# Kernel optimization log

Measured on AMD Instinct MI355X. Metric: run time of the kernel, lower is better.

## Reference

```python
import jax, jax.numpy as jnp
from jax import lax
import numpy as np

B, C, H, W = 16, 16, 256, 256
NOISE = 4
HID = 128
CDIM = 64
NCLS = 32
STEP_SIZE = 0.1
FIN = 3 * C + NOISE  # 52


def _lin(k, fin, fout, scale=None):
    # torch nn.Linear default init: U(-1/sqrt(fin), 1/sqrt(fin))
    s = (1.0 / np.sqrt(fin)) if scale is None else scale
    kw, kb = jax.random.split(k)
    w = jax.random.uniform(kw, (fin, fout), minval=-s, maxval=s, dtype=jnp.float32)
    b = jax.random.uniform(kb, (fout,), minval=-s, maxval=s, dtype=jnp.float32)
    return w, b


def setup_inputs() -> dict:
    key = jax.random.key(0)
    ks = jax.random.split(key, 8)
    x = jax.random.normal(ks[0], (B, C, H, W), dtype=jnp.float32)
    cond = jax.random.randint(ks[1], (B,), 0, NCLS)
    embed_tab = jax.random.normal(ks[2], (NCLS, CDIM), dtype=jnp.float32)
    film1_w, film1_b = _lin(ks[3], CDIM, 2 * HID)
    film2_w, film2_b = _lin(ks[4], CDIM, 2 * HID)
    fc1_w, fc1_b = _lin(ks[5], FIN, HID)
    fc2_w, fc2_b = _lin(ks[6], HID, HID)
    # original zero-inits fc3 (degenerate); use small random instead
    fc3_w, fc3_b = _lin(ks[7], HID, C, scale=0.02)
    return dict(x=x, cond=cond, embed_tab=embed_tab,
                film1_w=film1_w, film1_b=film1_b,
                film2_w=film2_w, film2_b=film2_b,
                fc1_w=fc1_w, fc1_b=fc1_b, fc2_w=fc2_w, fc2_b=fc2_b,
                fc3_w=fc3_w, fc3_b=fc3_b, n_steps=1)


def _dwconv(v, k2d):
    # depthwise 3x3 'same' conv, NCHW / OIHW
    kern = jnp.broadcast_to(k2d, (C, 1, 3, 3)).astype(v.dtype)
    return lax.conv_general_dilated(v, kern, (1, 1), 'SAME', feature_group_count=C)


def reference(x, cond, embed_tab, film1_w, film1_b, film2_w, film2_b,
              fc1_w, fc1_b, fc2_w, fc2_b, fc3_w, fc3_b, n_steps):
    sobel_x = jnp.array([[-1., 0., 1.], [-2., 0., 2.], [-1., 0., 1.]], jnp.float32)
    sobel_y = sobel_x.T
    emb = embed_tab[cond]                       # [B, CDIM]
    f1 = emb @ film1_w + film1_b                # [B, 2*HID]
    gamma1, beta1 = f1[:, :HID], f1[:, HID:]
    f2 = emb @ film2_w + film2_b
    gamma2, beta2 = f2[:, :HID], f2[:, HID:]
    for t in range(n_steps):
        gx = _dwconv(x, sobel_x)
        gy = _dwconv(x, sobel_y)
        noise = jax.random.normal(jax.random.fold_in(jax.random.key(1), t),
                                  (B, NOISE, H, W), dtype=x.dtype)
        feats = jnp.concatenate([x, gx, gy, noise], axis=1).transpose(0, 2, 3, 1)  # [B,H,W,FIN]
        h = jax.nn.relu(feats @ fc1_w + fc1_b)
        h = gamma1[:, None, None, :] * h + beta1[:, None, None, :]
        h = jax.nn.relu(h @ fc2_w + fc2_b)
        h = gamma2[:, None, None, :] * h + beta2[:, None, None, :]
        dx = (h @ fc3_w + fc3_b).transpose(0, 3, 1, 2)  # [B,C,H,W]
        dx = jnp.clip(dx, -10.0, 10.0)
        x = x + dx * STEP_SIZE
    return x
```

## Files before the change

### kernel.cpp

```cpp
#include <hip/hip_runtime.h>
#include <hip/hip_bf16.h>

using short8 = __attribute__((ext_vector_type(8))) short;
using f32x4  = __attribute__((ext_vector_type(4))) float;

constexpr int Bn = 16, Cc = 16, Hh = 256, Ww = 256;
constexpr int NOISEC = 4, HID = 128, CDIM = 64;
constexpr unsigned NTOT = (unsigned)Bn * NOISEC * Hh * Ww;
constexpr unsigned HALF = NTOT / 2;

__host__ __device__ __forceinline__ unsigned rotl(unsigned x, int d) {
    return (x << d) | (x >> (32 - d));
}

__host__ __device__ __forceinline__ void tf2x32(unsigned k0, unsigned k1,
                                                unsigned c0, unsigned c1,
                                                unsigned& o0, unsigned& o1) {
    unsigned k2 = k0 ^ k1 ^ 0x1BD11BDAu;
    unsigned x0 = c0 + k0, x1 = c1 + k1;
    x0 += x1; x1 = rotl(x1, 13); x1 ^= x0;
    x0 += x1; x1 = rotl(x1, 15); x1 ^= x0;
    x0 += x1; x1 = rotl(x1, 26); x1 ^= x0;
    x0 += x1; x1 = rotl(x1, 6);  x1 ^= x0;
    x0 += k1; x1 += k2 + 1u;
    x0 += x1; x1 = rotl(x1, 17); x1 ^= x0;
    x0 += x1; x1 = rotl(x1, 29); x1 ^= x0;
    x0 += x1; x1 = rotl(x1, 16); x1 ^= x0;
    x0 += x1; x1 = rotl(x1, 24); x1 ^= x0;
    x0 += k2; x1 += k0 + 2u;
    x0 += x1; x1 = rotl(x1, 13); x1 ^= x0;
    x0 += x1; x1 = rotl(x1, 15); x1 ^= x0;
    x0 += x1; x1 = rotl(x1, 26); x1 ^= x0;
    x0 += x1; x1 = rotl(x1, 6);  x1 ^= x0;
    x0 += k0; x1 += k1 + 3u;
    x0 += x1; x1 = rotl(x1, 17); x1 ^= x0;
    x0 += x1; x1 = rotl(x1, 29); x1 ^= x0;
    x0 += x1; x1 = rotl(x1, 16); x1 ^= x0;
    x0 += x1; x1 = rotl(x1, 24); x1 ^= x0;
    x0 += k1; x1 += k2 + 4u;
    x0 += x1; x1 = rotl(x1, 13); x1 ^= x0;
    x0 += x1; x1 = rotl(x1, 15); x1 ^= x0;
    x0 += x1; x1 = rotl(x1, 26); x1 ^= x0;
    x0 += x1; x1 = rotl(x1, 6);  x1 ^= x0;
    x0 += k2; x1 += k0 + 5u;
    o0 = x0; o1 = x1;
}

__device__ __forceinline__ float erfinv_f(float x) {
    float w = -log1pf(-x * x);
    float p;
    if (w < 5.0f) {
        w = w - 2.5f;
        p = 2.81022636e-08f;
        p = fmaf(p, w, 3.43273939e-07f);
        p = fmaf(p, w, -3.5233877e-06f);
        p = fmaf(p, w, -4.39150654e-06f);
        p = fmaf(p, w, 0.00021858087f);
        p = fmaf(p, w, -0.00125372503f);
        p = fmaf(p, w, -0.00417768164f);
        p = fmaf(p, w, 0.246640727f);
        p = fmaf(p, w, 1.50140941f);
    } else {
        w = sqrtf(w) - 3.0f;
        p = -0.000200214257f;
        p = fmaf(p, w, 0.000100950558f);
        p = fmaf(p, w, 0.00134934322f);
        p = fmaf(p, w, -0.00367342844f);
        p = fmaf(p, w, 0.00573950773f);
        p = fmaf(p, w, -0.0076224613f);
        p = fmaf(p, w, 0.00943887047f);
        p = fmaf(p, w, 1.00167406f);
        p = fmaf(p, w, 2.83297682f);
    }
    return p * x;
}

__device__ __forceinline__ float noise_val(unsigned j, unsigned fk0, unsigned fk1) {
    unsigned i = (j < HALF) ? j : (j - HALF);
    unsigned o0, o1;
    tf2x32(fk0, fk1, i, i + HALF, o0, o1);
    unsigned bits = (j < HALF) ? o0 : o1;
    unsigned fb = (bits >> 9) | 0x3F800000u;
    float f = __uint_as_float(fb) - 1.0f;
    const float lo = -0.99999994f;
    float u = f * 2.0f + lo;
    u = fmaxf(lo, u);
    return 1.4142135381698608f * erfinv_f(u);
}

__device__ __forceinline__ ushort f2bf(float f) {
    unsigned u = __float_as_uint(f);
    unsigned r = (u + 0x7FFFu + ((u >> 16) & 1u)) >> 16;
    return (ushort)r;
}

__device__ __forceinline__ unsigned cvtpk(float lo, float hi) {
    unsigned r;
    asm volatile("v_cvt_pk_bf16_f32 %0, %1, %2" : "=v"(r) : "v"(lo), "v"(hi));
    return r;
}

__device__ __forceinline__ unsigned rsw(int row) {
    return ((unsigned)((row ^ (row >> 4)) & 15)) << 4;
}

__global__ void film_kernel(const int* __restrict__ cond,
                            const float* __restrict__ embed,
                            const float* __restrict__ f1w, const float* __restrict__ f1b,
                            const float* __restrict__ f2w, const float* __restrict__ f2b,
                            float* __restrict__ film) {
    int b = blockIdx.x;
    int j = threadIdx.x;
    __shared__ float emb[CDIM];
    if (j < CDIM) emb[j] = embed[(size_t)cond[b] * CDIM + j];
    __syncthreads();
    float a1 = f1b[j], a2 = f2b[j];
    for (int c = 0; c < CDIM; ++c) {
        float e = emb[c];
        a1 += e * f1w[c * 2 * HID + j];
        a2 += e * f2w[c * 2 * HID + j];
    }
    int which = j >> 7;
    int idx = j & 127;
    float* fb_ = film + (size_t)b * 4 * HID;
    fb_[which * HID + idx] = a1;
    fb_[(2 + which) * HID + idx] = a2;
}

__global__ void prep_weights(const float* __restrict__ fc1w,
                             const float* __restrict__ fc2w,
                             const float* __restrict__ fc3w,
                             ushort* __restrict__ w1t, ushort* __restrict__ w2t,
                             ushort* __restrict__ w3t) {
    int i = blockIdx.x * 256 + threadIdx.x;
    if (i < 128 * 64) {
        int j = i >> 6, k = i & 63;
        w1t[i] = (k < 52) ? f2bf(fc1w[k * HID + j]) : (ushort)0;
    } else if (i < 8192 + 128 * 128) {
        int m = i - 8192;
        int j = m >> 7, k = m & 127;
        w2t[m] = f2bf(fc2w[k * HID + j]);
    } else if (i < 8192 + 16384 + 16 * 128) {
        int m = i - 24576;
        int c = m >> 7, k = m & 127;
        w3t[m] = f2bf(fc3w[k * Cc + c]);
    }
}

__global__ __launch_bounds__(256, 2)
void nca_mfma(const float* __restrict__ x,
              const ushort* __restrict__ w1t, const ushort* __restrict__ w2t,
              const ushort* __restrict__ w3t,
              const float* __restrict__ fc1b, const float* __restrict__ fc2b,
              const float* __restrict__ fc3b, const float* __restrict__ film,
              float* __restrict__ out, unsigned fk0, unsigned fk1) {
    __shared__ __align__(16) unsigned char Hb[256 * 256];

    const int blk = blockIdx.x, b = blk >> 8, y = blk & 255;
    const int t = threadIdx.x;
    const float* xb = x + (size_t)b * Cc * Hh * Ww;

    {
        const int q  = t & 63;
        const int cq = t >> 6;
        const int px0 = q * 4;
        const bool okm = (y > 0), okp = (y < Hh - 1);
        const bool ql = (q > 0), qr = (q < 63);

        float vx[4][4], vgx[4][4], vgy[4][4];
        #pragma unroll
        for (int cc = 0; cc < 4; ++cc) {
            const int c = cq * 4 + cc;
            const float* base = xb + ((size_t)c * Hh + (size_t)y) * Ww + px0;
            const float4 fz = {0.f, 0.f, 0.f, 0.f};
            float4 rm = okm ? *(const float4*)(base - Ww) : fz;
            float4 rc = *(const float4*)(base);
            float4 rp = okp ? *(const float4*)(base + Ww) : fz;
            float mL = __shfl_up(rm.w, 1),  mR = __shfl_down(rm.x, 1);
            float cL = __shfl_up(rc.w, 1),  cR = __shfl_down(rc.x, 1);
            float pL = __shfl_up(rp.w, 1),  pR = __shfl_down(rp.x, 1);
            if (!ql) { mL = 0.f; cL = 0.f; pL = 0.f; }
            if (!qr) { mR = 0.f; cR = 0.f; pR = 0.f; }
            float am[6] = {mL, rm.x, rm.y, rm.z, rm.w, mR};
            float ac[6] = {cL, rc.x, rc.y, rc.z, rc.w, cR};
            float ap[6] = {pL, rp.x, rp.y, rp.z, rp.w, pR};
            #pragma unroll
            for (int i = 0; i < 4; ++i) {
                float a0 = am[i], a1 = am[i + 1], a2 = am[i + 2];
                float b0 = ac[i], b1 = ac[i + 1], b2 = ac[i + 2];
                float e0 = ap[i], e1 = ap[i + 1], e2 = ap[i + 2];
                vx[cc][i]  = b1;
                vgx[cc][i] = (a2 + 2.f * b2 + e2) - (a0 + 2.f * b0 + e0);
                vgy[cc][i] = (e0 + 2.f * e1 + e2) - (a0 + 2.f * a1 + a2);
            }
        }
        #pragma unroll
        for (int i = 0; i < 4; ++i) {
            const int row = px0 + i;
            const unsigned sw = rsw(row);
            unsigned char* rowp = Hb + row * 256;
            uint2 u;
            u.x = cvtpk(vx[0][i], vx[1][i]);  u.y = cvtpk(vx[2][i], vx[3][i]);
            *(uint2*)(rowp + ((128u + 8u * cq) ^ sw)) = u;
            u.x = cvtpk(vgx[0][i], vgx[1][i]); u.y = cvtpk(vgx[2][i], vgx[3][i]);
            *(uint2*)(rowp + ((160u + 8u * cq) ^ sw)) = u;
            u.x = cvtpk(vgy[0][i], vgy[1][i]); u.y = cvtpk(vgy[2][i], vgy[3][i]);
            *(uint2*)(rowp + ((192u + 8u * cq) ^ sw)) = u;
        }
        unsigned nbase = (((unsigned)(b * NOISEC + cq) * Hh + (unsigned)y) * Ww) + (unsigned)px0;
        #pragma unroll
        for (int i = 0; i < 4; ++i) {
            float nz = noise_val(nbase + (unsigned)i, fk0, fk1);
            const int row = px0 + i;
            const unsigned sw = rsw(row);
            *(ushort*)(Hb + row * 256 + (((224u ^ sw) + 2u * cq))) = f2bf(nz);
        }
        if (cq == 0) {
            #pragma unroll
            for (int i = 0; i < 4; ++i) {
                const int row = px0 + i;
                const unsigned sw = rsw(row);
                *(uint2*)(Hb + row * 256 + ((232u & 15u) + (224u ^ sw))) = (uint2){0u, 0u};
                *(uint4*)(Hb + row * 256 + (240u ^ sw)) = (uint4){0u, 0u, 0u, 0u};
            }
        }
    }
    __syncthreads();

    const int lane = t & 63, wv = t >> 6;
    const int q = lane >> 4, p = lane & 15;
    const int nt0 = wv * 4;

    unsigned swn[4];
    #pragma unroll
    for (int n = 0; n < 4; ++n) swn[n] = rsw((nt0 + n) * 16 + p);

    f32x4 acc[8][4];

    #pragma unroll
    for (int m = 0; m < 8; ++m)
        #pragma unroll
        for (int n = 0; n < 4; ++n) acc[m][n] = (f32x4){0.f, 0.f, 0.f, 0.f};

    #pragma unroll
    for (int ks = 0; ks < 2; ++ks) {
        short8 Bf[4];
        #pragma unroll
        for (int n = 0; n < 4; ++n) {
            int row = (nt0 + n) * 16 + p;
            Bf[n] = *(const short8*)(Hb + row * 256 +
                                     (((unsigned)(128 + ks * 64 + q * 16)) ^ swn[n]));
        }
        #pragma unroll
        for (int m = 0; m < 8; ++m) {
            short8 Af = *(const short8*)((const unsigned char*)w1t +
                                         (m * 16 + p) * 128 + ks * 64 + q * 16);
            #pragma unroll
            for (int n = 0; n < 4; ++n)
                acc[m][n] = __builtin_amdgcn_mfma_f32_16x16x32_bf16(Af, Bf[n], acc[m][n], 0, 0, 0);
        }
    }
    const float* flm = film + (size_t)b * 4 * HID;
    #pragma unroll
    for (int m = 0; m < 8; ++m) {
        int j0 = m * 16 + q * 4;
        float4 cb = *(const float4*)(fc1b + j0);
        float4 G  = *(const float4*)(flm + 0 * HID + j0);
        float4 Be = *(const float4*)(flm + 1 * HID + j0);
        #pragma unroll
        for (int n = 0; n < 4; ++n) {
            int row = (nt0 + n) * 16 + p;
            f32x4 a = acc[m][n];
            float v0 = G.x * fmaxf(a[0] + cb.x, 0.f) + Be.x;
            float v1 = G.y * fmaxf(a[1] + cb.y, 0.f) + Be.y;
            float v2 = G.z * fmaxf(a[2] + cb.z, 0.f) + Be.z;
            float v3 = G.w * fmaxf(a[3] + cb.w, 0.f) + Be.w;
            uint2 u2; u2.x = cvtpk(v0, v1); u2.y = cvtpk(v2, v3);
            *(uint2*)(Hb + row * 256 + (((unsigned)(m * 32 + q * 8)) ^ swn[n])) = u2;
        }
    }

    #pragma unroll
    for (int m = 0; m < 8; ++m)
        #pragma unroll
        for (int n = 0; n < 4; ++n) acc[m][n] = (f32x4){0.f, 0.f, 0.f, 0.f};

    #pragma unroll
    for (int ks = 0; ks < 4; ++ks) {
        short8 Bf[4];
        #pragma unroll
        for (int n = 0; n < 4; ++n) {
            int row = (nt0 + n) * 16 + p;
            Bf[n] = *(const short8*)(Hb + row * 256 +
                                     (((unsigned)(ks * 64 + q * 16)) ^ swn[n]));
        }
        #pragma unroll
        for (int m = 0; m < 8; ++m) {
            short8 Af = *(const short8*)((const unsigned char*)w2t +
                                         (m * 16 + p) * 256 + ks * 64 + q * 16);
            #pragma unroll
            for (int n = 0; n < 4; ++n)
                acc[m][n] = __builtin_amdgcn_mfma_f32_16x16x32_bf16(Af, Bf[n], acc[m][n], 0, 0, 0);
        }
    }
    #pragma unroll
    for (int m = 0; m < 8; ++m) {
        int j0 = m * 16 + q * 4;
        float4 cb = *(const float4*)(fc2b + j0);
        float4 G  = *(const float4*)(flm + 2 * HID + j0);
        float4 Be = *(const float4*)(flm + 3 * HID + j0);
        #pragma unroll
        for (int n = 0; n < 4; ++n) {
            int row = (nt0 + n) * 16 + p;
            f32x4 a = acc[m][n];
            float v0 = G.x * fmaxf(a[0] + cb.x, 0.f) + Be.x;
            float v1 = G.y * fmaxf(a[1] + cb.y, 0.f) + Be.y;
            float v2 = G.z * fmaxf(a[2] + cb.z, 0.f) + Be.z;
            float v3 = G.w * fmaxf(a[3] + cb.w, 0.f) + Be.w;
            uint2 u2; u2.x = cvtpk(v0, v1); u2.y = cvtpk(v2, v3);
            *(uint2*)(Hb + row * 256 + (((unsigned)(m * 32 + q * 8)) ^ swn[n])) = u2;
        }
    }

    f32x4 a3[4];
    #pragma unroll
    for (int n = 0; n < 4; ++n) a3[n] = (f32x4){0.f, 0.f, 0.f, 0.f};

    #pragma unroll
    for (int ks = 0; ks < 4; ++ks) {
        short8 Af = *(const short8*)((const unsigned char*)w3t +
                                     p * 256 + ks * 64 + q * 16);
        #pragma unroll
        for (int n = 0; n < 4; ++n) {
            int row = (nt0 + n) * 16 + p;
            short8 Bf = *(const short8*)(Hb + row * 256 +
                                         (((unsigned)(ks * 64 + q * 16)) ^ swn[n]));
            a3[n] = __builtin_amdgcn_mfma_f32_16x16x32_bf16(Af, Bf, a3[n], 0, 0, 0);
        }
    }
    {
        float4 c3 = *(const float4*)(fc3b + q * 4);
        float c3a[4] = {c3.x, c3.y, c3.z, c3.w};
        float* ob = out + (size_t)b * Cc * Hh * Ww;
        #pragma unroll
        for (int n = 0; n < 4; ++n) {
            int px = (nt0 + n) * 16 + p;
            #pragma unroll
            for (int r = 0; r < 4; ++r) {
                int c = q * 4 + r;
                float dx = a3[n][r] + c3a[r];
                dx = fminf(fmaxf(dx, -10.0f), 10.0f);
                size_t off = (size_t)c * Hh * Ww + (size_t)y * Ww + px;
                ob[off] = xb[off] + 0.1f * dx;
            }
        }
    }
}

extern "C" void kernel_launch(void* const* d_in, const int* in_sizes, int n_in,
                              void* d_out, int out_size, void* d_ws, size_t ws_size,
                              hipStream_t stream) {
    const float* x     = (const float*)d_in[0];
    const int*   cond  = (const int*)d_in[1];
    const float* embed = (const float*)d_in[2];
    const float* f1w   = (const float*)d_in[3];
    const float* f1b   = (const float*)d_in[4];
    const float* f2w   = (const float*)d_in[5];
    const float* f2b   = (const float*)d_in[6];
    const float* fc1w  = (const float*)d_in[7];
    const float* fc1b  = (const float*)d_in[8];
    const float* fc2w  = (const float*)d_in[9];
    const float* fc2b  = (const float*)d_in[10];
    const float* fc3w  = (const float*)d_in[11];
    const float* fc3b  = (const float*)d_in[12];
    float* out = (float*)d_out;

    float*  film = (float*)d_ws;
    ushort* w1t  = (ushort*)((char*)d_ws + 32768);
    ushort* w2t  = (ushort*)((char*)d_ws + 32768 + 16384);
    ushort* w3t  = (ushort*)((char*)d_ws + 32768 + 16384 + 32768);

    unsigned fk0, fk1;
    tf2x32(0u, 1u, 0u, 0u, fk0, fk1);

    film_kernel<<<Bn, 256, 0, stream>>>(cond, embed, f1w, f1b, f2w, f2b, film);
    prep_weights<<<(8192 + 16384 + 2048 + 255) / 256, 256, 0, stream>>>(
        fc1w, fc2w, fc3w, w1t, w2t, w3t);
    nca_mfma<<<Bn * Hh, 256, 0, stream>>>(x, w1t, w2t, w3t, fc1b, fc2b, fc3b,
                                          film, out, fk0, fk1);
}
```

Measured before the change: 187.9 us.

## Split each row into two half-row blocks to halve LDS and raise occupancy

```diff
diff --git a/kernel.cpp b/kernel.cpp
--- a/kernel.cpp
+++ b/kernel.cpp
@@ -147,30 +147,30 @@
     }
 }
 
-__global__ __launch_bounds__(256, 2)
+__global__ __launch_bounds__(256, 3)
 void nca_mfma(const float* __restrict__ x,
               const ushort* __restrict__ w1t, const ushort* __restrict__ w2t,
               const ushort* __restrict__ w3t,
               const float* __restrict__ fc1b, const float* __restrict__ fc2b,
               const float* __restrict__ fc3b, const float* __restrict__ film,
               float* __restrict__ out, unsigned fk0, unsigned fk1) {
-    __shared__ __align__(16) unsigned char Hb[256 * 256];
-
-    const int blk = blockIdx.x, b = blk >> 8, y = blk & 255;
+    __shared__ __align__(16) unsigned char Hb[128 * 256];
+
+    const int blk = blockIdx.x;
+    const int half = blk & 1, y = (blk >> 1) & 255, b = blk >> 9;
     const int t = threadIdx.x;
     const float* xb = x + (size_t)b * Cc * Hh * Ww;
 
     {
-        const int q  = t & 63;
-        const int cq = t >> 6;
-        const int px0 = q * 4;
+        const int pq = t & 31;
+        const int cp = t >> 5;
+        const int px0 = half * 128 + pq * 4;
         const bool okm = (y > 0), okp = (y < Hh - 1);
-        const bool ql = (q > 0), qr = (q < 63);
-
-        float vx[4][4], vgx[4][4], vgy[4][4];
-        #pragma unroll
-        for (int cc = 0; cc < 4; ++cc) {
-            const int c = cq * 4 + cc;
+
+        float vx[2][4], vgx[2][4], vgy[2][4];
+        #pragma unroll
+        for (int cc = 0; cc < 2; ++cc) {
+            const int c = cp * 2 + cc;
             const float* base = xb + ((size_t)c * Hh + (size_t)y) * Ww + px0;
             const float4 fz = {0.f, 0.f, 0.f, 0.f};
             float4 rm = okm ? *(const float4*)(base - Ww) : fz;
@@ -179,8 +179,20 @@
             float mL = __shfl_up(rm.w, 1),  mR = __shfl_down(rm.x, 1);
             float cL = __shfl_up(rc.w, 1),  cR = __shfl_down(rc.x, 1);
             float pL = __shfl_up(rp.w, 1),  pR = __shfl_down(rp.x, 1);
-            if (!ql) { mL = 0.f; cL = 0.f; pL = 0.f; }
-            if (!qr) { mR = 0.f; cR = 0.f; pR = 0.f; }
+            if (pq == 0) {
+                if (half) {
+                    mL = okm ? base[-Ww - 1] : 0.f;
+                    cL = base[-1];
+                    pL = okp ? base[Ww - 1] : 0.f;
+                } else { mL = 0.f; cL = 0.f; pL = 0.f; }
+            }
+            if (pq == 31) {
+                if (!half) {
+                    mR = okm ? base[-Ww + 4] : 0.f;
+                    cR = base[4];
+                    pR = okp ? base[Ww + 4] : 0.f;
+                } else { mR = 0.f; cR = 0.f; pR = 0.f; }
+            }
             float am[6] = {mL, rm.x, rm.y, rm.z, rm.w, mR};
             float ac[6] = {cL, rc.x, rc.y, rc.z, rc.w, cR};
             float ap[6] = {pL, rp.x, rp.y, rp.z, rp.w, pR};
@@ -196,31 +208,31 @@
         }
         #pragma unroll
         for (int i = 0; i < 4; ++i) {
-            const int row = px0 + i;
+            const int row = pq * 4 + i;
             const unsigned sw = rsw(row);
             unsigned char* rowp = Hb + row * 256;
-            uint2 u;
-            u.x = cvtpk(vx[0][i], vx[1][i]);  u.y = cvtpk(vx[2][i], vx[3][i]);
-            *(uint2*)(rowp + ((128u + 8u * cq) ^ sw)) = u;
-            u.x = cvtpk(vgx[0][i], vgx[1][i]); u.y = cvtpk(vgx[2][i], vgx[3][i]);
-            *(uint2*)(rowp + ((160u + 8u * cq) ^ sw)) = u;
-            u.x = cvtpk(vgy[0][i], vgy[1][i]); u.y = cvtpk(vgy[2][i], vgy[3][i]);
-            *(uint2*)(rowp + ((192u + 8u * cq) ^ sw)) = u;
-        }
-        unsigned nbase = (((unsigned)(b * NOISEC + cq) * Hh + (unsigned)y) * Ww) + (unsigned)px0;
-        #pragma unroll
-        for (int i = 0; i < 4; ++i) {
-            float nz = noise_val(nbase + (unsigned)i, fk0, fk1);
-            const int row = px0 + i;
-            const unsigned sw = rsw(row);
-            *(ushort*)(Hb + row * 256 + (((224u ^ sw) + 2u * cq))) = f2bf(nz);
-        }
-        if (cq == 0) {
+            *(unsigned*)(rowp + ((128u + 4u * cp) ^ sw)) = cvtpk(vx[0][i],  vx[1][i]);
+            *(unsigned*)(rowp + ((160u + 4u * cp) ^ sw)) = cvtpk(vgx[0][i], vgx[1][i]);
+            *(unsigned*)(rowp + ((192u + 4u * cp) ^ sw)) = cvtpk(vgy[0][i], vgy[1][i]);
+        }
+        {
+            const int nch = cp & 3, nph = cp >> 2;
+            unsigned nb_ = (((unsigned)(b * NOISEC + nch) * Hh + (unsigned)y) * Ww)
+                           + (unsigned)(half * 128 + pq * 4 + nph * 2);
+            #pragma unroll
+            for (int i = 0; i < 2; ++i) {
+                float nz = noise_val(nb_ + (unsigned)i, fk0, fk1);
+                const int row = pq * 4 + nph * 2 + i;
+                const unsigned sw = rsw(row);
+                *(ushort*)(Hb + row * 256 + ((224u ^ sw) + 2u * nch)) = f2bf(nz);
+            }
+        }
+        if (cp == 0) {
             #pragma unroll
             for (int i = 0; i < 4; ++i) {
-                const int row = px0 + i;
+                const int row = pq * 4 + i;
                 const unsigned sw = rsw(row);
-                *(uint2*)(Hb + row * 256 + ((232u & 15u) + (224u ^ sw))) = (uint2){0u, 0u};
+                *(uint2*)(Hb + row * 256 + ((224u ^ sw) + 8u)) = (uint2){0u, 0u};
                 *(uint4*)(Hb + row * 256 + (240u ^ sw)) = (uint4){0u, 0u, 0u, 0u};
             }
         }
@@ -229,24 +241,24 @@
 
     const int lane = t & 63, wv = t >> 6;
     const int q = lane >> 4, p = lane & 15;
-    const int nt0 = wv * 4;
-
-    unsigned swn[4];
-    #pragma unroll
-    for (int n = 0; n < 4; ++n) swn[n] = rsw((nt0 + n) * 16 + p);
-
-    f32x4 acc[8][4];
+    const int nt0 = wv * 2;
+
+    unsigned swn[2];
+    #pragma unroll
+    for (int n = 0; n < 2; ++n) swn[n] = rsw((nt0 + n) * 16 + p);
+
+    f32x4 acc[8][2];
 
     #pragma unroll
     for (int m = 0; m < 8; ++m)
         #pragma unroll
-        for (int n = 0; n < 4; ++n) acc[m][n] = (f32x4){0.f, 0.f, 0.f, 0.f};
+        for (int n = 0; n < 2; ++n) acc[m][n] = (f32x4){0.f, 0.f, 0.f, 0.f};
 
     #pragma unroll
     for (int ks = 0; ks < 2; ++ks) {
-        short8 Bf[4];
-        #pragma unroll
-        for (int n = 0; n < 4; ++n) {
+        short8 Bf[2];
+        #pragma unroll
+        for (int n = 0; n < 2; ++n) {
             int row = (nt0 + n) * 16 + p;
             Bf[n] = *(const short8*)(Hb + row * 256 +
                                      (((unsigned)(128 + ks * 64 + q * 16)) ^ swn[n]));
@@ -256,7 +268,7 @@
             short8 Af = *(const short8*)((const unsigned char*)w1t +
                                          (m * 16 + p) * 128 + ks * 64 + q * 16);
             #pragma unroll
-            for (int n = 0; n < 4; ++n)
+            for (int n = 0; n < 2; ++n)
                 acc[m][n] = __builtin_amdgcn_mfma_f32_16x16x32_bf16(Af, Bf[n], acc[m][n], 0, 0, 0);
         }
     }
@@ -268,7 +280,7 @@
         float4 G  = *(const float4*)(flm + 0 * HID + j0);
         float4 Be = *(const float4*)(flm + 1 * HID + j0);
         #pragma unroll
-        for (int n = 0; n < 4; ++n) {
+        for (int n = 0; n < 2; ++n) {
             int row = (nt0 + n) * 16 + p;
             f32x4 a = acc[m][n];
             float v0 = G.x * fmaxf(a[0] + cb.x, 0.f) + Be.x;
@@ -283,13 +295,13 @@
     #pragma unroll
     for (int m = 0; m < 8; ++m)
         #pragma unroll
-        for (int n = 0; n < 4; ++n) acc[m][n] = (f32x4){0.f, 0.f, 0.f, 0.f};
+        for (int n = 0; n < 2; ++n) acc[m][n] = (f32x4){0.f, 0.f, 0.f, 0.f};
 
     #pragma unroll
     for (int ks = 0; ks < 4; ++ks) {
-        short8 Bf[4];
-        #pragma unroll
-        for (int n = 0; n < 4; ++n) {
+        short8 Bf[2];
+        #pragma unroll
+        for (int n = 0; n < 2; ++n) {
             int row = (nt0 + n) * 16 + p;
             Bf[n] = *(const short8*)(Hb + row * 256 +
                                      (((unsigned)(ks * 64 + q * 16)) ^ swn[n]));
@@ -299,7 +311,7 @@
             short8 Af = *(const short8*)((const unsigned char*)w2t +
                                          (m * 16 + p) * 256 + ks * 64 + q * 16);
             #pragma unroll
-            for (int n = 0; n < 4; ++n)
+            for (int n = 0; n < 2; ++n)
                 acc[m][n] = __builtin_amdgcn_mfma_f32_16x16x32_bf16(Af, Bf[n], acc[m][n], 0, 0, 0);
         }
     }
@@ -310,7 +322,7 @@
         float4 G  = *(const float4*)(flm + 2 * HID + j0);
         float4 Be = *(const float4*)(flm + 3 * HID + j0);
         #pragma unroll
-        for (int n = 0; n < 4; ++n) {
+        for (int n = 0; n < 2; ++n) {
             int row = (nt0 + n) * 16 + p;
             f32x4 a = acc[m][n];
             float v0 = G.x * fmaxf(a[0] + cb.x, 0.f) + Be.x;
@@ -322,16 +334,16 @@
         }
     }
 
-    f32x4 a3[4];
-    #pragma unroll
-    for (int n = 0; n < 4; ++n) a3[n] = (f32x4){0.f, 0.f, 0.f, 0.f};
+    f32x4 a3[2];
+    #pragma unroll
+    for (int n = 0; n < 2; ++n) a3[n] = (f32x4){0.f, 0.f, 0.f, 0.f};
 
     #pragma unroll
     for (int ks = 0; ks < 4; ++ks) {
         short8 Af = *(const short8*)((const unsigned char*)w3t +
                                      p * 256 + ks * 64 + q * 16);
         #pragma unroll
-        for (int n = 0; n < 4; ++n) {
+        for (int n = 0; n < 2; ++n) {
             int row = (nt0 + n) * 16 + p;
             short8 Bf = *(const short8*)(Hb + row * 256 +
                                          (((unsigned)(ks * 64 + q * 16)) ^ swn[n]));
@@ -343,8 +355,8 @@
         float c3a[4] = {c3.x, c3.y, c3.z, c3.w};
         float* ob = out + (size_t)b * Cc * Hh * Ww;
         #pragma unroll
-        for (int n = 0; n < 4; ++n) {
-            int px = (nt0 + n) * 16 + p;
+        for (int n = 0; n < 2; ++n) {
+            int px = half * 128 + (nt0 + n) * 16 + p;
             #pragma unroll
             for (int r = 0; r < 4; ++r) {
                 int c = q * 4 + r;
@@ -386,6 +398,6 @@
     film_kernel<<<Bn, 256, 0, stream>>>(cond, embed, f1w, f1b, f2w, f2b, film);
     prep_weights<<<(8192 + 16384 + 2048 + 255) / 256, 256, 0, stream>>>(
         fc1w, fc2w, fc3w, w1t, w2t, w3t);
-    nca_mfma<<<Bn * Hh, 256, 0, stream>>>(x, w1t, w2t, w3t, fc1b, fc2b, fc3b,
-                                          film, out, fk0, fk1);
-}
+    nca_mfma<<<Bn * Hh * 2, 256, 0, stream>>>(x, w1t, w2t, w3t, fc1b, fc2b, fc3b,
+                                              film, out, fk0, fk1);
+}
```

Result: slower. 295.2 us (+57.1%).
